# Kernel tuning notes

Hardware: AMD Instinct MI355X
Metric: run time of the kernel (lower is better)

## Reference

```python
import jax, jax.numpy as jnp
import numpy as np

EPS = 1e-8      # laplace_transform epsilon
RC = 0.5        # residual_coff
L = 2           # num_layers
NU, NB, NI, D = 100000, 30000, 50000, 128
E_UB, E_UI, E_BI = 300000, 500000, 500000


def _l2norm(x):
    # F.normalize(x, p=2, dim=1)
    n = jnp.linalg.norm(x, axis=1, keepdims=True)
    return x / jnp.maximum(n, 1e-12)


def _spmm(rows, cols, vals, feats, n):
    # sparse (COO) matmul: out[r] += vals[e] * feats[cols[e]]
    return jax.ops.segment_sum(vals[:, None] * feats[cols], rows, num_segments=n)


def _sym_norm_graph(u, v, na, nb):
    # bipartite block matrix [[0, B],[B^T, 0]] with D^-1/2 A D^-1/2 normalization
    rows = jnp.concatenate([u, v + na])
    cols = jnp.concatenate([v + na, u])
    deg = jax.ops.segment_sum(jnp.ones(rows.shape[0], jnp.float32), rows,
                              num_segments=na + nb)
    dinv = 1.0 / (jnp.sqrt(deg) + EPS)
    vals = dinv[rows] * dinv[cols]
    return rows, cols, vals


def _one_propagate(rows, cols, vals, afeat, bfeat):
    n = afeat.shape[0] + bfeat.shape[0]
    feats = jnp.concatenate([afeat, bfeat], axis=0)
    ini = _l2norm(feats)
    acc = feats  # all_feats starts with raw feats, summed at the end
    for i in range(L):
        feats = _spmm(rows, cols, vals, feats, n)
        feats = (feats + RC * ini) / (i + 2)
        feats = _l2norm(feats)
        acc = acc + feats
    return acc[:afeat.shape[0]], acc[afeat.shape[0]:]


def setup_inputs() -> dict:
    key = jax.random.key(0)
    ks = jax.random.split(key, 10)
    return {
        "users_feat": jax.random.normal(ks[0], (NU, D), jnp.float32) * 0.1,
        "bundles_feat": jax.random.normal(ks[1], (NB, D), jnp.float32) * 0.1,
        "items_feat": jax.random.normal(ks[2], (NI, D), jnp.float32) * 0.1,
        "bi_vals": jax.random.uniform(ks[3], (E_BI,), jnp.float32),
        "ub_u": jax.random.randint(ks[4], (E_UB,), 0, NU),
        "ub_b": jax.random.randint(ks[5], (E_UB,), 0, NB),
        "ui_u": jax.random.randint(ks[6], (E_UI,), 0, NU),
        "ui_i": jax.random.randint(ks[7], (E_UI,), 0, NI),
        "bi_b": jax.random.randint(ks[8], (E_BI,), 0, NB),
        "bi_i": jax.random.randint(ks[9], (E_BI,), 0, NI),
    }


def reference(users_feat, bundles_feat, items_feat, bi_vals,
              ub_u, ub_b, ui_u, ui_i, bi_b, bi_i):
    nu, nb, ni = users_feat.shape[0], bundles_feat.shape[0], items_feat.shape[0]
    # UB (history) propagation
    r, c, v = _sym_norm_graph(ub_u, ub_b, nu, nb)
    hist_users, hist_bundles = _one_propagate(r, c, v, users_feat, bundles_feat)
    # UI (affinity) propagation
    r, c, v = _sym_norm_graph(ui_u, ui_i, nu, ni)
    aff_users, ui_items = _one_propagate(r, c, v, users_feat, items_feat)
    # BI aggregation: bundles x items sparse graph @ item features
    aff_bundles = _spmm(bi_b, bi_i, bi_vals, ui_items, nb)
    # concat [aff_users, hist_users, aff_bundles, hist_bundles] along rows
    return jnp.concatenate([aff_users, hist_users, aff_bundles, hist_bundles], axis=0)
```

## Files before the change

### kernel.cpp

```cpp
#include <hip/hip_runtime.h>

#define FD   128
#define FDH  64
#define EPSN 1e-8f
#define RCC  0.5f
#define SCAN_TPB 256
#define SCAN_ELEMS 1024

typedef unsigned int uint;
typedef unsigned short u16;
typedef float fx2 __attribute__((ext_vector_type(2)));

__device__ __forceinline__ float wave_sum(float x) {
#pragma unroll
    for (int off = 32; off > 0; off >>= 1) x += __shfl_xor(x, off);
    return x;
}

__device__ __forceinline__ uint packbf2(float a, float b) {
    uint ua = __float_as_uint(a); ua += 0x7fffu + ((ua >> 16) & 1u);
    uint ub = __float_as_uint(b); ub += 0x7fffu + ((ub >> 16) & 1u);
    return (ua >> 16) | (ub & 0xffff0000u);
}
__device__ __forceinline__ float2 unpackbf2(uint v) {
    return make_float2(__uint_as_float(v << 16), __uint_as_float(v & 0xffff0000u));
}
__device__ __forceinline__ fx2 unpackfp8(uint v) {
    return __builtin_amdgcn_cvt_pk_f32_fp8((int)v, false);
}
__device__ __forceinline__ u16 packfp8(float a, float b) {
    return (u16)__builtin_amdgcn_cvt_pk_fp8_f32(a, b, 0, false);
}

__global__ void passA(const int* __restrict__ ub_u, const int* __restrict__ ub_b,
                      const int* __restrict__ ui_u, const int* __restrict__ ui_i,
                      const int* __restrict__ bi_b, const int* __restrict__ bi_i,
                      const float* __restrict__ uf, const float* __restrict__ bf,
                      const float* __restrict__ itf,
                      int E_UB, int E_UI, int E_BI, int NU, int NB, int n1, int n2, int NT,
                      int nblk_edges,
                      int* __restrict__ head, int2* __restrict__ pairLL,
                      uint* __restrict__ fini16, float* __restrict__ normf) {
    if ((int)blockIdx.x < nblk_edges) {
        int e = blockIdx.x * blockDim.x + threadIdx.x;
        if (e < E_UB) {
            int a = ub_u[e], b = ub_b[e] + NU;
            int s0 = 2 * e;
            int p0 = atomicExch(&head[a], s0);
            int p1 = atomicExch(&head[b], s0 + 1);
            ((int4*)pairLL)[e] = make_int4(p0, b, p1, a);
        } else if (e < E_UB + E_UI) {
            int f = e - E_UB;
            int a = ui_u[f], bl = ui_i[f] + NU;
            int s0 = 2 * E_UB + 2 * f;
            int p0 = atomicExch(&head[n1 + a], s0);
            int p1 = atomicExch(&head[n1 + bl], s0 + 1);
            ((int4*)pairLL)[E_UB + f] = make_int4(p0, bl, p1, a);
        } else if (e < E_UB + E_UI + E_BI) {
            int g = e - E_UB - E_UI;
            int s = 2 * E_UB + 2 * E_UI + g;
            int p = atomicExch(&head[n1 + n2 + bi_b[g]], s);
            pairLL[s] = make_int2(p, bi_i[g]);
        }
    } else {
        int w = (((int)blockIdx.x - nblk_edges) * blockDim.x + threadIdx.x) >> 6;
        int lane = threadIdx.x & 63;
        if (w >= NT) return;
        const float* src = (w < NU) ? uf + (size_t)w * FD
                         : (w < NU + NB) ? bf + (size_t)(w - NU) * FD
                         : itf + (size_t)(w - NU - NB) * FD;
        float2 x = ((const float2*)src)[lane];
        float ss = wave_sum(x.x * x.x + x.y * x.y);
        float nrm = sqrtf(ss);
        float inv = 1.0f / fmaxf(nrm, 1e-12f);
        fini16[(size_t)w * FDH + lane] = packbf2(x.x * inv, x.y * inv);
        if (lane == 0) normf[w] = nrm;
    }
}

__global__ void passB(const int* __restrict__ head, const int2* __restrict__ pairLL,
                      int NN, int n12, int* __restrict__ deg, float* __restrict__ dinv) {
    int r = blockIdx.x * blockDim.x + threadIdx.x;
    if (r > NN) return;
    if (r == NN) { deg[NN] = 0; return; }
    int c = 0;
    int s = head[r];
    while (s >= 0) { c++; s = pairLL[s].x; }
    deg[r] = c;
    if (r < n12) dinv[r] = 1.0f / (sqrtf((float)c) + EPSN);
}

__global__ void conv_g8(const uint* __restrict__ fini16, const float* __restrict__ normf,
                        const float* __restrict__ dinv,
                        int n1, int NU, int NB, int n12, u16* __restrict__ g8) {
    int w = (blockIdx.x * blockDim.x + threadIdx.x) >> 6;
    int lane = threadIdx.x & 63;
    if (w >= n12) return;
    int node = (w < n1) ? w : ((w - n1 < NU) ? (w - n1) : (w - n1 + NB));
    float sc = dinv[w] * normf[node];
    float2 f = unpackbf2(fini16[(size_t)node * FDH + lane]);
    g8[(size_t)w * FDH + lane] = packfp8(f.x * sc, f.y * sc);
}

__global__ void scan_a(const int* __restrict__ in, int* __restrict__ out,
                       int* __restrict__ bsum, int nelem) {
    __shared__ int tsum[SCAN_TPB];
    int tid = threadIdx.x;
    int base = blockIdx.x * SCAN_ELEMS + tid * 4;
    int v0 = (base + 0 < nelem) ? in[base + 0] : 0;
    int v1 = (base + 1 < nelem) ? in[base + 1] : 0;
    int v2 = (base + 2 < nelem) ? in[base + 2] : 0;
    int v3 = (base + 3 < nelem) ? in[base + 3] : 0;
    int s = v0 + v1 + v2 + v3;
    tsum[tid] = s;
    __syncthreads();
    for (int off = 1; off < SCAN_TPB; off <<= 1) {
        int y = (tid >= off) ? tsum[tid - off] : 0;
        __syncthreads();
        tsum[tid] += y;
        __syncthreads();
    }
    int excl = tsum[tid] - s;
    if (tid == SCAN_TPB - 1) bsum[blockIdx.x] = tsum[SCAN_TPB - 1];
    if (base + 0 < nelem) out[base + 0] = excl;
    excl += v0;
    if (base + 1 < nelem) out[base + 1] = excl;
    excl += v1;
    if (base + 2 < nelem) out[base + 2] = excl;
    excl += v2;
    if (base + 3 < nelem) out[base + 3] = excl;
}

__global__ void scan_b(int* __restrict__ bsum, int nb) {
    __shared__ int sm[512];
    int tid = threadIdx.x;
    int v = (tid < nb) ? bsum[tid] : 0;
    sm[tid] = v;
    __syncthreads();
    for (int off = 1; off < 512; off <<= 1) {
        int y = (tid >= off) ? sm[tid - off] : 0;
        __syncthreads();
        sm[tid] += y;
        __syncthreads();
    }
    if (tid < nb) bsum[tid] = sm[tid] - v;
}

__global__ void scan_c(int* __restrict__ out, const int* __restrict__ bsum, int nelem) {
    int base = blockIdx.x * SCAN_ELEMS + threadIdx.x * 4;
    int add = bsum[blockIdx.x];
#pragma unroll
    for (int k = 0; k < 4; ++k)
        if (base + k < nelem) out[base + k] += add;
}

__global__ void passC(const int* __restrict__ head, const int2* __restrict__ pairLL,
                      const int* __restrict__ rowptr, const float* __restrict__ bi_vals,
                      int NN, int n12, int S1,
                      int* __restrict__ cols, float* __restrict__ wts) {
    int r = blockIdx.x * blockDim.x + threadIdx.x;
    if (r >= NN) return;
    int pos = rowptr[r];
    int s = head[r];
    if (r < n12) {
        while (s >= 0) { int2 p = pairLL[s]; cols[pos++] = p.y; s = p.x; }
    } else {
        while (s >= 0) {
            int2 p = pairLL[s];
            cols[pos] = p.y;
            wts[pos - S1] = bi_vals[s - S1];
            pos++; s = p.x;
        }
    }
}

__global__ void spmm_L1(const int* __restrict__ rowptr, const int* __restrict__ cols,
                        const float* __restrict__ dinv, const float* __restrict__ normf,
                        const uint* __restrict__ fini16, const u16* __restrict__ g8,
                        uint* __restrict__ facc16, u16* __restrict__ fX8,
                        int n1, int NU, int NB, int n12) {
    int w = (blockIdx.x * blockDim.x + threadIdx.x) >> 6;
    int lane = threadIdx.x & 63;
    if (w >= n12) return;
    int s = rowptr[w], e = rowptr[w + 1];
    bool ui = (w >= n1);
    int sB = ui ? n1 : 0;
    int node = ui ? ((w - n1 < NU) ? (w - n1) : (w - n1 + NB)) : w;
    float dr = dinv[w];
    const u16* tab = g8 + (size_t)sB * FDH + lane;
    float ax = 0.0f, ay = 0.0f;
    int j = s;
    for (; j + 4 <= e; j += 4) {
        int c0 = cols[j], c1 = cols[j + 1], c2 = cols[j + 2], c3 = cols[j + 3];
        uint x0 = tab[(size_t)c0 * FDH];
        uint x1 = tab[(size_t)c1 * FDH];
        uint x2 = tab[(size_t)c2 * FDH];
        uint x3 = tab[(size_t)c3 * FDH];
        fx2 f0 = unpackfp8(x0), f1 = unpackfp8(x1);
        fx2 f2 = unpackfp8(x2), f3 = unpackfp8(x3);
        ax += f0.x + f1.x + f2.x + f3.x;
        ay += f0.y + f1.y + f2.y + f3.y;
    }
    for (; j < e; ++j) {
        fx2 f0 = unpackfp8(tab[(size_t)cols[j] * FDH]);
        ax += f0.x; ay += f0.y;
    }
    float2 i0 = unpackbf2(fini16[(size_t)node * FDH + lane]);
    float vx = (dr * ax + RCC * i0.x) * 0.5f;
    float vy = (dr * ay + RCC * i0.y) * 0.5f;
    float ss = wave_sum(vx * vx + vy * vy);
    float inv = 1.0f / fmaxf(sqrtf(ss), 1e-12f);
    vx *= inv; vy *= inv;
    float nr = normf[node];
    facc16[(size_t)w * FDH + lane] = packbf2(fmaf(i0.x, nr, vx), fmaf(i0.y, nr, vy));
    fX8[(size_t)w * FDH + lane] = packfp8(vx * dr, vy * dr);
}

__global__ void spmm_L2(const int* __restrict__ rowptr, const int* __restrict__ cols,
                        const float* __restrict__ dinv, const uint* __restrict__ fini16,
                        const uint* __restrict__ facc16, const u16* __restrict__ fX8,
                        uint* __restrict__ items16, float* __restrict__ outp,
                        int n1, int NU, int NB, int n12) {
    int w = (blockIdx.x * blockDim.x + threadIdx.x) >> 6;
    int lane = threadIdx.x & 63;
    if (w >= n12) return;
    int s = rowptr[w], e = rowptr[w + 1];
    bool ui = (w >= n1);
    int sB = ui ? n1 : 0;
    int node = ui ? ((w - n1 < NU) ? (w - n1) : (w - n1 + NB)) : w;
    float dr = dinv[w];
    const u16* tab = fX8 + (size_t)sB * FDH + lane;
    float ax = 0.0f, ay = 0.0f;
    int j = s;
    for (; j + 4 <= e; j += 4) {
        int c0 = cols[j], c1 = cols[j + 1], c2 = cols[j + 2], c3 = cols[j + 3];
        uint x0 = tab[(size_t)c0 * FDH];
        uint x1 = tab[(size_t)c1 * FDH];
        uint x2 = tab[(size_t)c2 * FDH];
        uint x3 = tab[(size_t)c3 * FDH];
        fx2 f0 = unpackfp8(x0), f1 = unpackfp8(x1);
        fx2 f2 = unpackfp8(x2), f3 = unpackfp8(x3);
        ax += f0.x + f1.x + f2.x + f3.x;
        ay += f0.y + f1.y + f2.y + f3.y;
    }
    for (; j < e; ++j) {
        fx2 f0 = unpackfp8(tab[(size_t)cols[j] * FDH]);
        ax += f0.x; ay += f0.y;
    }
    float2 i0 = unpackbf2(fini16[(size_t)node * FDH + lane]);
    float vx = (dr * ax + RCC * i0.x) * (1.0f / 3.0f);
    float vy = (dr * ay + RCC * i0.y) * (1.0f / 3.0f);
    float ss = wave_sum(vx * vx + vy * vy);
    float inv = 1.0f / fmaxf(sqrtf(ss), 1e-12f);
    vx *= inv; vy *= inv;
    float2 a0 = unpackbf2(facc16[(size_t)w * FDH + lane]);
    float anx = a0.x + vx, any = a0.y + vy;
    if (!ui) {
        size_t dst = (w < NU) ? (size_t)(NU + w) : (size_t)(2 * NU + NB + (w - NU));
        ((float2*)(outp + dst * FD))[lane] = make_float2(anx, any);
    } else {
        int l = w - n1;
        if (l < NU) ((float2*)(outp + (size_t)l * FD))[lane] = make_float2(anx, any);
        else        items16[(size_t)(l - NU) * FDH + lane] = packbf2(anx, any);
    }
}

__global__ void bi_gather(const int* __restrict__ rowptr, const int* __restrict__ cols,
                          const float* __restrict__ wts, int S1,
                          const uint* __restrict__ items16,
                          float* __restrict__ outb, int nb) {
    int w = (blockIdx.x * blockDim.x + threadIdx.x) >> 6;
    int lane = threadIdx.x & 63;
    if (w >= nb) return;
    int s = rowptr[w], e = rowptr[w + 1];
    float ax = 0.0f, ay = 0.0f;
    int j = s;
    for (; j + 4 <= e; j += 4) {
        int c0 = cols[j], c1 = cols[j + 1], c2 = cols[j + 2], c3 = cols[j + 3];
        float w0 = wts[j - S1], w1 = wts[j + 1 - S1];
        float w2 = wts[j + 2 - S1], w3 = wts[j + 3 - S1];
        uint x0 = items16[(size_t)c0 * FDH + lane];
        uint x1 = items16[(size_t)c1 * FDH + lane];
        uint x2 = items16[(size_t)c2 * FDH + lane];
        uint x3 = items16[(size_t)c3 * FDH + lane];
        float2 f0 = unpackbf2(x0), f1 = unpackbf2(x1);
        float2 f2 = unpackbf2(x2), f3 = unpackbf2(x3);
        ax = fmaf(w0, f0.x, ax); ay = fmaf(w0, f0.y, ay);
        ax = fmaf(w1, f1.x, ax); ay = fmaf(w1, f1.y, ay);
        ax = fmaf(w2, f2.x, ax); ay = fmaf(w2, f2.y, ay);
        ax = fmaf(w3, f3.x, ax); ay = fmaf(w3, f3.y, ay);
    }
    for (; j < e; ++j) {
        float w0 = wts[j - S1];
        float2 f0 = unpackbf2(items16[(size_t)cols[j] * FDH + lane]);
        ax = fmaf(w0, f0.x, ax); ay = fmaf(w0, f0.y, ay);
    }
    ((float2*)(outb + (size_t)w * FD))[lane] = make_float2(ax, ay);
}

extern "C" void kernel_launch(void* const* d_in, const int* in_sizes, int n_in,
                              void* d_out, int out_size, void* d_ws, size_t ws_size,
                              hipStream_t stream) {
    const float* users   = (const float*)d_in[0];
    const float* bundles = (const float*)d_in[1];
    const float* items   = (const float*)d_in[2];
    const float* bi_vals = (const float*)d_in[3];
    const int* ub_u = (const int*)d_in[4];
    const int* ub_b = (const int*)d_in[5];
    const int* ui_u = (const int*)d_in[6];
    const int* ui_i = (const int*)d_in[7];
    const int* bi_b = (const int*)d_in[8];
    const int* bi_i = (const int*)d_in[9];

    const int NU = in_sizes[0] / FD;
    const int NB = in_sizes[1] / FD;
    const int NI = in_sizes[2] / FD;
    const int E_BI = in_sizes[3];
    const int E_UB = in_sizes[4];
    const int E_UI = in_sizes[6];
    float* out = (float*)d_out;

    const int n1 = NU + NB, n2 = NU + NI;
    const int n12 = n1 + n2;
    const int NT = NU + NB + NI;
    const int NN = n12 + NB;
    const int S1 = 2 * E_UB + 2 * E_UI;
    const int TOT = S1 + E_BI;
    const int ETOT = E_UB + E_UI + E_BI;

    uint* fini16   = (uint*)d_ws;
    uint* facc16   = fini16 + (size_t)NT * FDH;
    uint* items16  = facc16 + (size_t)n12 * FDH;
    u16* g8        = (u16*)(items16 + (size_t)NI * FDH);
    u16* fX8       = g8 + (size_t)n12 * FDH;
    float* normf   = (float*)(fX8 + (size_t)n12 * FDH);
    float* dinv    = normf + NT;
    float* wts     = dinv + n12;
    int* deg       = (int*)(wts + E_BI);
    int* rowptr    = deg + (NN + 1);
    int* head      = rowptr + (NN + 1);
    int* bsum      = head + NN;
    int* cols      = bsum + 512;
    int2* pairLL   = (int2*)((((size_t)(cols + TOT)) + 15) & ~(size_t)15);

    dim3 blk(256);
    auto rows_grid = [](int n) { return dim3((unsigned)((n + 3) / 4)); };
    auto thr_grid  = [](int n) { return dim3((unsigned)((n + 255) / 256)); };

    hipMemsetAsync(head, 0xFF, (size_t)NN * 4, stream);
    int nblk_edges = (ETOT + 255) / 256;
    int nblk_prep  = (NT + 3) / 4;
    passA<<<dim3((unsigned)(nblk_edges + nblk_prep)), blk, 0, stream>>>(
        ub_u, ub_b, ui_u, ui_i, bi_b, bi_i, users, bundles, items,
        E_UB, E_UI, E_BI, NU, NB, n1, n2, NT, nblk_edges,
        head, pairLL, fini16, normf);
    passB<<<thr_grid(NN + 1), blk, 0, stream>>>(head, pairLL, NN, n12, deg, dinv);
    conv_g8<<<rows_grid(n12), blk, 0, stream>>>(fini16, normf, dinv, n1, NU, NB, n12, g8);
    {
        int nelem = NN + 1;
        int nblk = (nelem + SCAN_ELEMS - 1) / SCAN_ELEMS;
        scan_a<<<dim3((unsigned)nblk), dim3(SCAN_TPB), 0, stream>>>(deg, rowptr, bsum, nelem);
        scan_b<<<dim3(1), dim3(512), 0, stream>>>(bsum, nblk);
        scan_c<<<dim3((unsigned)nblk), dim3(SCAN_TPB), 0, stream>>>(rowptr, bsum, nelem);
    }
    passC<<<thr_grid(NN), blk, 0, stream>>>(head, pairLL, rowptr, bi_vals,
                                            NN, n12, S1, cols, wts);

    spmm_L1<<<rows_grid(n12), blk, 0, stream>>>(rowptr, cols, dinv, normf,
                                                fini16, g8, facc16, fX8, n1, NU, NB, n12);
    spmm_L2<<<rows_grid(n12), blk, 0, stream>>>(rowptr, cols, dinv, fini16,
                                                facc16, fX8, items16, out, n1, NU, NB, n12);
    bi_gather<<<rows_grid(NB), blk, 0, stream>>>(rowptr + n12, cols, wts, S1, items16,
        out + (size_t)2 * NU * FD, NB);
}
```

Baseline: 724.7 us.

## Split each wave into two half-waves gathering alternate edges with wider loads

```diff
diff --git a/kernel.cpp b/kernel.cpp
--- a/kernel.cpp
+++ b/kernel.cpp
@@ -9,6 +9,7 @@
 
 typedef unsigned int uint;
 typedef unsigned short u16;
+typedef unsigned char u8;
 typedef float fx2 __attribute__((ext_vector_type(2)));
 
 __device__ __forceinline__ float wave_sum(float x) {
@@ -24,9 +25,6 @@
 }
 __device__ __forceinline__ float2 unpackbf2(uint v) {
     return make_float2(__uint_as_float(v << 16), __uint_as_float(v & 0xffff0000u));
-}
-__device__ __forceinline__ fx2 unpackfp8(uint v) {
-    return __builtin_amdgcn_cvt_pk_f32_fp8((int)v, false);
 }
 __device__ __forceinline__ u16 packfp8(float a, float b) {
     return (u16)__builtin_amdgcn_cvt_pk_fp8_f32(a, b, 0, false);
@@ -163,105 +161,141 @@
     int pos = rowptr[r];
     int s = head[r];
     if (r < n12) {
-        while (s >= 0) { int2 p = pairLL[s]; cols[pos++] = p.y; s = p.x; }
+        while (s >= 0) { int2 p = pairLL[s]; cols[pos++] = p.y << 7; s = p.x; }
     } else {
         while (s >= 0) {
             int2 p = pairLL[s];
-            cols[pos] = p.y;
+            cols[pos] = p.y << 8;
             wts[pos - S1] = bi_vals[s - S1];
             pos++; s = p.x;
         }
     }
 }
 
+#define GATHER_FP8(TAB)                                                          \
+    float a0 = 0.f, a1 = 0.f, a2 = 0.f, a3 = 0.f;                                \
+    {                                                                            \
+        int j = s;                                                               \
+        for (; j + 8 <= e; j += 8) {                                             \
+            int o0 = cols[j + h], o1 = cols[j + 2 + h];                          \
+            int o2 = cols[j + 4 + h], o3 = cols[j + 6 + h];                      \
+            uint x0 = *(const uint*)(TAB + o0);                                  \
+            uint x1 = *(const uint*)(TAB + o1);                                  \
+            uint x2 = *(const uint*)(TAB + o2);                                  \
+            uint x3 = *(const uint*)(TAB + o3);                                  \
+            fx2 p0 = __builtin_amdgcn_cvt_pk_f32_fp8((int)x0, false);            \
+            fx2 r0 = __builtin_amdgcn_cvt_pk_f32_fp8((int)x0, true);             \
+            fx2 p1 = __builtin_amdgcn_cvt_pk_f32_fp8((int)x1, false);            \
+            fx2 r1 = __builtin_amdgcn_cvt_pk_f32_fp8((int)x1, true);             \
+            fx2 p2 = __builtin_amdgcn_cvt_pk_f32_fp8((int)x2, false);            \
+            fx2 r2 = __builtin_amdgcn_cvt_pk_f32_fp8((int)x2, true);             \
+            fx2 p3 = __builtin_amdgcn_cvt_pk_f32_fp8((int)x3, false);            \
+            fx2 r3 = __builtin_amdgcn_cvt_pk_f32_fp8((int)x3, true);             \
+            a0 += p0.x + p1.x + p2.x + p3.x;                                     \
+            a1 += p0.y + p1.y + p2.y + p3.y;                                     \
+            a2 += r0.x + r1.x + r2.x + r3.x;                                     \
+            a3 += r0.y + r1.y + r2.y + r3.y;                                     \
+        }                                                                        \
+        for (; j + 2 <= e; j += 2) {                                             \
+            int o = cols[j + h];                                                 \
+            uint x = *(const uint*)(TAB + o);                                    \
+            fx2 p = __builtin_amdgcn_cvt_pk_f32_fp8((int)x, false);              \
+            fx2 r = __builtin_amdgcn_cvt_pk_f32_fp8((int)x, true);               \
+            a0 += p.x; a1 += p.y; a2 += r.x; a3 += r.y;                          \
+        }                                                                        \
+        if (j < e && h == 0) {                                                   \
+            int o = cols[j];                                                     \
+            uint x = *(const uint*)(TAB + o);                                    \
+            fx2 p = __builtin_amdgcn_cvt_pk_f32_fp8((int)x, false);              \
+            fx2 r = __builtin_amdgcn_cvt_pk_f32_fp8((int)x, true);               \
+            a0 += p.x; a1 += p.y; a2 += r.x; a3 += r.y;                          \
+        }                                                                        \
+    }                                                                            \
+    a0 += __shfl_xor(a0, 32); a1 += __shfl_xor(a1, 32);                          \
+    a2 += __shfl_xor(a2, 32); a3 += __shfl_xor(a3, 32);
+
 __global__ void spmm_L1(const int* __restrict__ rowptr, const int* __restrict__ cols,
                         const float* __restrict__ dinv, const float* __restrict__ normf,
                         const uint* __restrict__ fini16, const u16* __restrict__ g8,
-                        uint* __restrict__ facc16, u16* __restrict__ fX8,
+                        uint* __restrict__ facc16, uint* __restrict__ fX8,
                         int n1, int NU, int NB, int n12) {
     int w = (blockIdx.x * blockDim.x + threadIdx.x) >> 6;
     int lane = threadIdx.x & 63;
     if (w >= n12) return;
+    int h = lane >> 5, q = lane & 31;
     int s = rowptr[w], e = rowptr[w + 1];
     bool ui = (w >= n1);
-    int sB = ui ? n1 : 0;
     int node = ui ? ((w - n1 < NU) ? (w - n1) : (w - n1 + NB)) : w;
     float dr = dinv[w];
-    const u16* tab = g8 + (size_t)sB * FDH + lane;
-    float ax = 0.0f, ay = 0.0f;
-    int j = s;
-    for (; j + 4 <= e; j += 4) {
-        int c0 = cols[j], c1 = cols[j + 1], c2 = cols[j + 2], c3 = cols[j + 3];
-        uint x0 = tab[(size_t)c0 * FDH];
-        uint x1 = tab[(size_t)c1 * FDH];
-        uint x2 = tab[(size_t)c2 * FDH];
-        uint x3 = tab[(size_t)c3 * FDH];
-        fx2 f0 = unpackfp8(x0), f1 = unpackfp8(x1);
-        fx2 f2 = unpackfp8(x2), f3 = unpackfp8(x3);
-        ax += f0.x + f1.x + f2.x + f3.x;
-        ay += f0.y + f1.y + f2.y + f3.y;
-    }
-    for (; j < e; ++j) {
-        fx2 f0 = unpackfp8(tab[(size_t)cols[j] * FDH]);
-        ax += f0.x; ay += f0.y;
-    }
-    float2 i0 = unpackbf2(fini16[(size_t)node * FDH + lane]);
-    float vx = (dr * ax + RCC * i0.x) * 0.5f;
-    float vy = (dr * ay + RCC * i0.y) * 0.5f;
-    float ss = wave_sum(vx * vx + vy * vy);
-    float inv = 1.0f / fmaxf(sqrtf(ss), 1e-12f);
-    vx *= inv; vy *= inv;
-    float nr = normf[node];
-    facc16[(size_t)w * FDH + lane] = packbf2(fmaf(i0.x, nr, vx), fmaf(i0.y, nr, vy));
-    fX8[(size_t)w * FDH + lane] = packfp8(vx * dr, vy * dr);
+    const u8* tab = (const u8*)g8 + ((size_t)(ui ? n1 : 0) << 7) + (q << 2);
+    GATHER_FP8(tab)
+    uint2 iu = ((const uint2*)(fini16 + (size_t)node * FDH))[q];
+    float2 i01 = unpackbf2(iu.x), i23 = unpackbf2(iu.y);
+    float v0 = (dr * a0 + RCC * i01.x) * 0.5f;
+    float v1 = (dr * a1 + RCC * i01.y) * 0.5f;
+    float v2 = (dr * a2 + RCC * i23.x) * 0.5f;
+    float v3 = (dr * a3 + RCC * i23.y) * 0.5f;
+    float sq = v0 * v0 + v1 * v1 + v2 * v2 + v3 * v3;
+#pragma unroll
+    for (int off = 16; off > 0; off >>= 1) sq += __shfl_xor(sq, off);
+    float inv = 1.0f / fmaxf(sqrtf(sq), 1e-12f);
+    v0 *= inv; v1 *= inv; v2 *= inv; v3 *= inv;
+    if (h == 0) {
+        float nr = normf[node];
+        uint2 fa;
+        fa.x = packbf2(fmaf(i01.x, nr, v0), fmaf(i01.y, nr, v1));
+        fa.y = packbf2(fmaf(i23.x, nr, v2), fmaf(i23.y, nr, v3));
+        ((uint2*)(facc16 + (size_t)w * FDH))[q] = fa;
+        int xu = __builtin_amdgcn_cvt_pk_fp8_f32(v0 * dr, v1 * dr, 0, false);
+        xu = __builtin_amdgcn_cvt_pk_fp8_f32(v2 * dr, v3 * dr, xu, true);
+        fX8[(size_t)w * 32 + q] = (uint)xu;
+    }
 }
 
 __global__ void spmm_L2(const int* __restrict__ rowptr, const int* __restrict__ cols,
                         const float* __restrict__ dinv, const uint* __restrict__ fini16,
-                        const uint* __restrict__ facc16, const u16* __restrict__ fX8,
+                        const uint* __restrict__ facc16, const uint* __restrict__ fX8,
                         uint* __restrict__ items16, float* __restrict__ outp,
                         int n1, int NU, int NB, int n12) {
     int w = (blockIdx.x * blockDim.x + threadIdx.x) >> 6;
     int lane = threadIdx.x & 63;
     if (w >= n12) return;
+    int h = lane >> 5, q = lane & 31;
     int s = rowptr[w], e = rowptr[w + 1];
     bool ui = (w >= n1);
-    int sB = ui ? n1 : 0;
     int node = ui ? ((w - n1 < NU) ? (w - n1) : (w - n1 + NB)) : w;
     float dr = dinv[w];
-    const u16* tab = fX8 + (size_t)sB * FDH + lane;
-    float ax = 0.0f, ay = 0.0f;
-    int j = s;
-    for (; j + 4 <= e; j += 4) {
-        int c0 = cols[j], c1 = cols[j + 1], c2 = cols[j + 2], c3 = cols[j + 3];
-        uint x0 = tab[(size_t)c0 * FDH];
-        uint x1 = tab[(size_t)c1 * FDH];
-        uint x2 = tab[(size_t)c2 * FDH];
-        uint x3 = tab[(size_t)c3 * FDH];
-        fx2 f0 = unpackfp8(x0), f1 = unpackfp8(x1);
-        fx2 f2 = unpackfp8(x2), f3 = unpackfp8(x3);
-        ax += f0.x + f1.x + f2.x + f3.x;
-        ay += f0.y + f1.y + f2.y + f3.y;
-    }
-    for (; j < e; ++j) {
-        fx2 f0 = unpackfp8(tab[(size_t)cols[j] * FDH]);
-        ax += f0.x; ay += f0.y;
-    }
-    float2 i0 = unpackbf2(fini16[(size_t)node * FDH + lane]);
-    float vx = (dr * ax + RCC * i0.x) * (1.0f / 3.0f);
-    float vy = (dr * ay + RCC * i0.y) * (1.0f / 3.0f);
-    float ss = wave_sum(vx * vx + vy * vy);
-    float inv = 1.0f / fmaxf(sqrtf(ss), 1e-12f);
-    vx *= inv; vy *= inv;
-    float2 a0 = unpackbf2(facc16[(size_t)w * FDH + lane]);
-    float anx = a0.x + vx, any = a0.y + vy;
-    if (!ui) {
-        size_t dst = (w < NU) ? (size_t)(NU + w) : (size_t)(2 * NU + NB + (w - NU));
-        ((float2*)(outp + dst * FD))[lane] = make_float2(anx, any);
-    } else {
-        int l = w - n1;
-        if (l < NU) ((float2*)(outp + (size_t)l * FD))[lane] = make_float2(anx, any);
-        else        items16[(size_t)(l - NU) * FDH + lane] = packbf2(anx, any);
+    const u8* tab = (const u8*)fX8 + ((size_t)(ui ? n1 : 0) << 7) + (q << 2);
+    GATHER_FP8(tab)
+    uint2 iu = ((const uint2*)(fini16 + (size_t)node * FDH))[q];
+    float2 i01 = unpackbf2(iu.x), i23 = unpackbf2(iu.y);
+    float v0 = (dr * a0 + RCC * i01.x) * (1.0f / 3.0f);
+    float v1 = (dr * a1 + RCC * i01.y) * (1.0f / 3.0f);
+    float v2 = (dr * a2 + RCC * i23.x) * (1.0f / 3.0f);
+    float v3 = (dr * a3 + RCC * i23.y) * (1.0f / 3.0f);
+    float sq = v0 * v0 + v1 * v1 + v2 * v2 + v3 * v3;
+#pragma unroll
+    for (int off = 16; off > 0; off >>= 1) sq += __shfl_xor(sq, off);
+    float inv = 1.0f / fmaxf(sqrtf(sq), 1e-12f);
+    v0 *= inv; v1 *= inv; v2 *= inv; v3 *= inv;
+    uint2 au = ((const uint2*)(facc16 + (size_t)w * FDH))[q];
+    float2 a01 = unpackbf2(au.x), a23 = unpackbf2(au.y);
+    float n0 = a01.x + v0, o1v = a01.y + v1, n2v = a23.x + v2, n3 = a23.y + v3;
+    if (h == 0) {
+        if (!ui) {
+            size_t dst = (w < NU) ? (size_t)(NU + w) : (size_t)(2 * NU + NB + (w - NU));
+            ((float4*)(outp + dst * FD))[q] = make_float4(n0, o1v, n2v, n3);
+        } else {
+            int l = w - n1;
+            if (l < NU) {
+                ((float4*)(outp + (size_t)l * FD))[q] = make_float4(n0, o1v, n2v, n3);
+            } else {
+                uint2 it;
+                it.x = packbf2(n0, o1v);
+                it.y = packbf2(n2v, n3);
+                ((uint2*)(items16 + (size_t)(l - NU) * FDH))[q] = it;
+            }
+        }
     }
 }
 
@@ -272,30 +306,50 @@
     int w = (blockIdx.x * blockDim.x + threadIdx.x) >> 6;
     int lane = threadIdx.x & 63;
     if (w >= nb) return;
+    int h = lane >> 5, q = lane & 31;
     int s = rowptr[w], e = rowptr[w + 1];
-    float ax = 0.0f, ay = 0.0f;
+    const u8* tab = (const u8*)items16 + (q << 3);
+    float a0 = 0.f, a1 = 0.f, a2 = 0.f, a3 = 0.f;
     int j = s;
-    for (; j + 4 <= e; j += 4) {
-        int c0 = cols[j], c1 = cols[j + 1], c2 = cols[j + 2], c3 = cols[j + 3];
-        float w0 = wts[j - S1], w1 = wts[j + 1 - S1];
-        float w2 = wts[j + 2 - S1], w3 = wts[j + 3 - S1];
-        uint x0 = items16[(size_t)c0 * FDH + lane];
-        uint x1 = items16[(size_t)c1 * FDH + lane];
-        uint x2 = items16[(size_t)c2 * FDH + lane];
-        uint x3 = items16[(size_t)c3 * FDH + lane];
-        float2 f0 = unpackbf2(x0), f1 = unpackbf2(x1);
-        float2 f2 = unpackbf2(x2), f3 = unpackbf2(x3);
-        ax = fmaf(w0, f0.x, ax); ay = fmaf(w0, f0.y, ay);
-        ax = fmaf(w1, f1.x, ax); ay = fmaf(w1, f1.y, ay);
-        ax = fmaf(w2, f2.x, ax); ay = fmaf(w2, f2.y, ay);
-        ax = fmaf(w3, f3.x, ax); ay = fmaf(w3, f3.y, ay);
-    }
-    for (; j < e; ++j) {
-        float w0 = wts[j - S1];
-        float2 f0 = unpackbf2(items16[(size_t)cols[j] * FDH + lane]);
-        ax = fmaf(w0, f0.x, ax); ay = fmaf(w0, f0.y, ay);
-    }
-    ((float2*)(outb + (size_t)w * FD))[lane] = make_float2(ax, ay);
+    for (; j + 8 <= e; j += 8) {
+        int o0 = cols[j + h], o1 = cols[j + 2 + h];
+        int o2 = cols[j + 4 + h], o3 = cols[j + 6 + h];
+        float w0 = wts[j + h - S1], w1 = wts[j + 2 + h - S1];
+        float w2 = wts[j + 4 + h - S1], w3 = wts[j + 6 + h - S1];
+        uint2 x0 = *(const uint2*)(tab + o0);
+        uint2 x1 = *(const uint2*)(tab + o1);
+        uint2 x2 = *(const uint2*)(tab + o2);
+        uint2 x3 = *(const uint2*)(tab + o3);
+        float2 f; 
+        f = unpackbf2(x0.x); a0 = fmaf(w0, f.x, a0); a1 = fmaf(w0, f.y, a1);
+        f = unpackbf2(x0.y); a2 = fmaf(w0, f.x, a2); a3 = fmaf(w0, f.y, a3);
+        f = unpackbf2(x1.x); a0 = fmaf(w1, f.x, a0); a1 = fmaf(w1, f.y, a1);
+        f = unpackbf2(x1.y); a2 = fmaf(w1, f.x, a2); a3 = fmaf(w1, f.y, a3);
+        f = unpackbf2(x2.x); a0 = fmaf(w2, f.x, a0); a1 = fmaf(w2, f.y, a1);
+        f = unpackbf2(x2.y); a2 = fmaf(w2, f.x, a2); a3 = fmaf(w2, f.y, a3);
+        f = unpackbf2(x3.x); a0 = fmaf(w3, f.x, a0); a1 = fmaf(w3, f.y, a1);
+        f = unpackbf2(x3.y); a2 = fmaf(w3, f.x, a2); a3 = fmaf(w3, f.y, a3);
+    }
+    for (; j + 2 <= e; j += 2) {
+        int o = cols[j + h];
+        float wt = wts[j + h - S1];
+        uint2 x = *(const uint2*)(tab + o);
+        float2 f;
+        f = unpackbf2(x.x); a0 = fmaf(wt, f.x, a0); a1 = fmaf(wt, f.y, a1);
+        f = unpackbf2(x.y); a2 = fmaf(wt, f.x, a2); a3 = fmaf(wt, f.y, a3);
+    }
+    if (j < e && h == 0) {
+        int o = cols[j];
+        float wt = wts[j - S1];
+        uint2 x = *(const uint2*)(tab + o);
+        float2 f;
+        f = unpackbf2(x.x); a0 = fmaf(wt, f.x, a0); a1 = fmaf(wt, f.y, a1);
+        f = unpackbf2(x.y); a2 = fmaf(wt, f.x, a2); a3 = fmaf(wt, f.y, a3);
+    }
+    a0 += __shfl_xor(a0, 32); a1 += __shfl_xor(a1, 32);
+    a2 += __shfl_xor(a2, 32); a3 += __shfl_xor(a3, 32);
+    if (h == 0)
+        ((float4*)(outb + (size_t)w * FD))[q] = make_float4(a0, a1, a2, a3);
 }
 
 extern "C" void kernel_launch(void* const* d_in, const int* in_sizes, int n_in,
@@ -332,8 +386,8 @@
     uint* facc16   = fini16 + (size_t)NT * FDH;
     uint* items16  = facc16 + (size_t)n12 * FDH;
     u16* g8        = (u16*)(items16 + (size_t)NI * FDH);
-    u16* fX8       = g8 + (size_t)n12 * FDH;
-    float* normf   = (float*)(fX8 + (size_t)n12 * FDH);
+    uint* fX8      = (uint*)(g8 + (size_t)n12 * FDH);
+    float* normf   = (float*)(fX8 + (size_t)n12 * 32);
     float* dinv    = normf + NT;
     float* wts     = dinv + n12;
     int* deg       = (int*)(wts + E_BI);
```

Result: no change. 718.2 us (-0.9%).
